# Kernel optimization log

Measured on AMD Instinct MI355X. Metric: run time of the kernel, lower is better.

## Reference

```python
import jax, jax.numpy as jnp
import numpy as np

IN_SZ = 256
OUT_SZ = 256
N_CHAN = 1024
RANK = 4  # min(4, IN_SZ*OUT_SZ)
B = 256
N = 2048


def setup_inputs() -> dict:
    key = jax.random.key(0)
    k_x, k_idx, k_u, k_v, k_b = jax.random.split(key, 5)
    x = jax.random.normal(k_x, (B, N, IN_SZ), dtype=jnp.float32)
    indices = jax.random.randint(k_idx, (B,), 0, N_CHAN)
    # init per reset_parameters(const=1.0)
    bound_u = np.sqrt(3.0 / RANK)              # fan_out of weights_U [C, r] is r
    weights_U = jax.random.uniform(k_u, (N_CHAN, RANK), jnp.float32, -bound_u, bound_u)
    bound_v = np.sqrt(1.0 / (IN_SZ * OUT_SZ))  # fan_out of weights_V [r, in*out]
    weights_V = jax.random.uniform(k_v, (RANK, IN_SZ * OUT_SZ), jnp.float32, -bound_v, bound_v)
    bound_b = np.sqrt(1.0 / RANK)
    bias = jax.random.uniform(k_b, (N_CHAN, 1, OUT_SZ), jnp.float32, -bound_b, bound_b)
    return {"x": x, "indices": indices, "weights_U": weights_U,
            "weights_V": weights_V, "bias": bias}


def reference(x, indices, weights_U, weights_V, bias):
    # weight synthesis: gather U rows first, then low-rank expand (same math as
    # full (U@V)[indices], without materializing unused channels)
    w = (weights_U[indices] @ weights_V).reshape(-1, IN_SZ, OUT_SZ)  # [B, in, out]
    out = jnp.einsum('bni,bio->bno', x, w)                            # [B, N, out]
    out = out + bias[indices]                                         # [B,1,out] broadcast
    return out
```

## Files before the change

kernel.cpp:

```cpp
#include <hip/hip_runtime.h>
#include <cstdint>

#define AS1 __attribute__((address_space(1)))
#define AS3 __attribute__((address_space(3)))

typedef __attribute__((ext_vector_type(8))) short short8;
typedef __attribute__((ext_vector_type(4))) float f32x4;

constexpr int SEQ   = 2048;
constexpr int INSZ  = 256;
constexpr int OUTSZ = 256;

__device__ __forceinline__ ushort f2bf(float f) {
  union { float f; uint32_t u; } v; v.f = f;
  uint32_t u = v.u;
  return (ushort)((u + 0x7FFFu + ((u >> 16) & 1u)) >> 16);
}
__device__ __forceinline__ uint32_t pk2(float a, float b) {
  return (uint32_t)f2bf(a) | ((uint32_t)f2bf(b) << 16);
}
__device__ __forceinline__ uint32_t cvtpk(float lo, float hi) {
  uint32_t r;
  asm("v_cvt_pk_bf16_f32 %0, %1, %2" : "=v"(r) : "v"(lo), "v"(hi));
  return r;
}

__global__ __launch_bounds__(256) void synth_w(
    const float* __restrict__ U, const float* __restrict__ V,
    const int* __restrict__ idx, ushort* __restrict__ wsW)
{
  const int b   = blockIdx.y;
  const int kb  = blockIdx.x;
  const int tid = threadIdx.x;
  const int ch  = idx[b];
  const float u0 = U[ch*4+0], u1 = U[ch*4+1], u2 = U[ch*4+2], u3 = U[ch*4+3];

  __shared__ ushort tile[64][260];

  const int o4    = (tid & 63) * 4;
  const int kbase = (tid >> 6) * 16;
  for (int kk = 0; kk < 16; ++kk) {
    const int k  = kbase + kk;
    const int gk = kb*64 + k;
    const float* vp = V + (size_t)gk*OUTSZ + o4;
    float4 a = *(const float4*)(vp);
    float4 c = *(const float4*)(vp + 65536);
    float4 d = *(const float4*)(vp + 131072);
    float4 e = *(const float4*)(vp + 196608);
    ushort4 pkv;
    pkv.x = f2bf(u0*a.x + u1*c.x + u2*d.x + u3*e.x);
    pkv.y = f2bf(u0*a.y + u1*c.y + u2*d.y + u3*e.y);
    pkv.z = f2bf(u0*a.z + u1*c.z + u2*d.z + u3*e.z);
    pkv.w = f2bf(u0*a.w + u1*c.w + u2*d.w + u3*e.w);
    *(ushort4*)(&tile[k][o4]) = pkv;
  }
  __syncthreads();

  for (int s = 0; s < 8; ++s) {
    const int c      = s*256 + tid;
    const int kshalf = c >> 10;
    const int nb     = (c >> 6) & 15;
    const int lane   = c & 63;
    const int o      = nb*16 + (lane & 15);
    const int k0     = kshalf*32 + (lane >> 4)*8;
    uint4 pkv;
    pkv.x = (uint32_t)tile[k0+0][o] | ((uint32_t)tile[k0+1][o] << 16);
    pkv.y = (uint32_t)tile[k0+2][o] | ((uint32_t)tile[k0+3][o] << 16);
    pkv.z = (uint32_t)tile[k0+4][o] | ((uint32_t)tile[k0+5][o] << 16);
    pkv.w = (uint32_t)tile[k0+6][o] | ((uint32_t)tile[k0+7][o] << 16);
    uint4* dst = (uint4*)(wsW + (size_t)b*65536 + (size_t)(2*kb + kshalf)*8192
                              + nb*512 + lane*8);
    *dst = pkv;
  }
}

__global__ __launch_bounds__(256, 4) void lr_gemm(
    const float* __restrict__ x, const int* __restrict__ idx,
    const float* __restrict__ bias, const ushort* __restrict__ wsW,
    float* __restrict__ out)
{
  __shared__ float ldsF[4][64*32];

  const int wg  = blockIdx.x;
  const int swz = (wg & 7) * 1024 + (wg >> 3);
  const int b   = swz >> 5;
  const int n0  = (swz & 31) * 64;

  const int tid  = threadIdx.x;
  const int lane = tid & 63;
  const int wave = tid >> 6;
  const int hi16 = lane >> 4;
  const int lo16 = lane & 15;

  const float*  xb  = x + ((size_t)b*SEQ + n0)*INSZ;
  const ushort* wbp = wsW + (size_t)b*65536 + wave*2048 + lane*8;

  const int csrc = (lane & 7) ^ (lane >> 3);
#define STAGE(S) do {                                                        \
    _Pragma("unroll")                                                        \
    for (int t = 0; t < 2; ++t) {                                            \
      const int g = wave*2 + t;                        \
      const int r = g*8 + (lane >> 3);                                       \
      const float* srcp = xb + (size_t)r*INSZ + (S)*32 + csrc*4;             \
      float* dstp = &ldsF[(S) & 3][g*256];                                   \
      __builtin_amdgcn_global_load_lds((const AS1 void*)srcp,                \
                                       (AS3 void*)dstp, 16, 0, 0);           \
    } } while (0)

  STAGE(0); STAGE(1); STAGE(2);
  asm volatile("s_waitcnt vmcnt(4)" ::: "memory");
  __builtin_amdgcn_s_barrier();
  __builtin_amdgcn_sched_barrier(0);

  f32x4 acc[4][4] = {};
  const int s0idx = (hi16*2) ^ (lo16 & 7);
  const int s1idx = s0idx ^ 1;

#define KSTEP(S, WSTR) do {                                                  \
    short8 bf[4], af[4];                                                     \
    _Pragma("unroll")                                                        \
    for (int n = 0; n < 4; ++n)                                              \
      bf[n] = *(const short8*)(wbp + (size_t)(S)*8192 + n*512);              \
    if ((S) < 5) STAGE((S)+3);                                               \
    const float* fb = &ldsF[(S) & 3][0];                                     \
    _Pragma("unroll")                                                        \
    for (int m = 0; m < 4; ++m) {                                            \
      const float* p = fb + (m*16 + lo16)*32;                                \
      float4 fa = *(const float4*)(p + s0idx*4);                             \
      float4 fc = *(const float4*)(p + s1idx*4);                             \
      union { uint32_t u[4]; short8 s8; } pk;                                \
      pk.u[0] = cvtpk(fa.x, fa.y); pk.u[1] = cvtpk(fa.z, fa.w);              \
      pk.u[2] = cvtpk(fc.x, fc.y); pk.u[3] = cvtpk(fc.z, fc.w);              \
      af[m] = pk.s8;                                                         \
    }                                                                        \
    _Pragma("unroll")                                                        \
    for (int m = 0; m < 4; ++m)                                              \
      _Pragma("unroll")                                                      \
      for (int n = 0; n < 4; ++n)                                            \
        acc[m][n] = __builtin_amdgcn_mfma_f32_16x16x32_bf16(                 \
            bf[n], af[m], acc[m][n], 0, 0, 0);                               \
    if ((S) < 7) {                                                           \
      __builtin_amdgcn_sched_barrier(0);                                     \
      asm volatile("s_waitcnt vmcnt(" WSTR ")" ::: "memory");                \
      __builtin_amdgcn_s_barrier();                                          \
      __builtin_amdgcn_sched_barrier(0);                                     \
    } } while (0)

  KSTEP(0, "4"); KSTEP(1, "4"); KSTEP(2, "4"); KSTEP(3, "4");
  KSTEP(4, "4"); KSTEP(5, "2"); KSTEP(6, "0"); KSTEP(7, "0");

  const int ch = idx[b];
  float* outb = out + ((size_t)b*SEQ + n0)*OUTSZ;
  #pragma unroll
  for (int n = 0; n < 4; ++n) {
    const float4 bv4 = *(const float4*)(bias + (size_t)ch*OUTSZ
                                        + wave*64 + n*16 + hi16*4);
    #pragma unroll
    for (int m = 0; m < 4; ++m) {
      float4 v;
      v.x = acc[m][n][0] + bv4.x;
      v.y = acc[m][n][1] + bv4.y;
      v.z = acc[m][n][2] + bv4.z;
      v.w = acc[m][n][3] + bv4.w;
      *(float4*)(outb + (size_t)(m*16 + lo16)*OUTSZ
                 + wave*64 + n*16 + hi16*4) = v;
    }
  }
#undef KSTEP
#undef STAGE
}

extern "C" void kernel_launch(void* const* d_in, const int* in_sizes, int n_in,
                              void* d_out, int out_size, void* d_ws, size_t ws_size,
                              hipStream_t stream) {
  const float* x    = (const float*)d_in[0];
  const int*   idx  = (const int*)d_in[1];
  const float* U    = (const float*)d_in[2];
  const float* V    = (const float*)d_in[3];
  const float* bias = (const float*)d_in[4];
  float* out  = (float*)d_out;
  ushort* wsW = (ushort*)d_ws;

  synth_w<<<dim3(4, 256), 256, 0, stream>>>(U, V, idx, wsW);
  lr_gemm<<<8192, 256, 0, stream>>>(x, idx, bias, wsW, out);
}
```

Measured before the change: 255.7 us.

## Deepen GEMM prefetch pipeline with 8 LDS stages and rotating B registers

The lr_gemm kernel now gives each of the 8 K-steps its own LDS buffer (64 KB total) and issues six x-tile stages up front instead of three. The bf16 weight fragments are loaded three steps ahead into four rotating register sets, with vmcnt thresholds retuned to match. The goal is to hide more global-load latency behind MFMA work. In exchange, occupancy drops: launch bounds go from 4 to 2 blocks per CU, and the larger LDS and register footprint limits resident waves.

Measured after the change: 260.2 us. Within noise of the previous version (+1.8%).

```diff
diff --git a/kernel.cpp b/kernel.cpp
--- a/kernel.cpp
+++ b/kernel.cpp
@@ -74,12 +74,12 @@
   }
 }
 
-__global__ __launch_bounds__(256, 4) void lr_gemm(
+__global__ __launch_bounds__(256, 2) void lr_gemm(
     const float* __restrict__ x, const int* __restrict__ idx,
     const float* __restrict__ bias, const ushort* __restrict__ wsW,
     float* __restrict__ out)
 {
-  __shared__ float ldsF[4][64*32];
+  __shared__ float ldsF[8][2048];
 
   const int wg  = blockIdx.x;
   const int swz = (wg & 7) * 1024 + (wg >> 3);
@@ -102,13 +102,23 @@
       const int g = wave*2 + t;                        \
       const int r = g*8 + (lane >> 3);                                       \
       const float* srcp = xb + (size_t)r*INSZ + (S)*32 + csrc*4;             \
-      float* dstp = &ldsF[(S) & 3][g*256];                                   \
+      float* dstp = &ldsF[(S)][g*256];                                       \
       __builtin_amdgcn_global_load_lds((const AS1 void*)srcp,                \
                                        (AS3 void*)dstp, 16, 0, 0);           \
     } } while (0)
 
-  STAGE(0); STAGE(1); STAGE(2);
-  asm volatile("s_waitcnt vmcnt(4)" ::: "memory");
+#define LOADB(DST, S) do {                                                   \
+    _Pragma("unroll")                                                        \
+    for (int n = 0; n < 4; ++n)                                              \
+      DST[n] = *(const short8*)(wbp + (size_t)(S)*8192 + n*512);             \
+    } while (0)
+
+  short8 bfA[4], bfB[4], bfC[4];
+  short8 bfD[4];
+
+  LOADB(bfA, 0); LOADB(bfB, 1); LOADB(bfC, 2);
+  STAGE(0); STAGE(1); STAGE(2); STAGE(3); STAGE(4); STAGE(5);
+  asm volatile("s_waitcnt vmcnt(10)" ::: "memory");
   __builtin_amdgcn_s_barrier();
   __builtin_amdgcn_sched_barrier(0);
 
@@ -116,13 +126,11 @@
   const int s0idx = (hi16*2) ^ (lo16 & 7);
   const int s1idx = s0idx ^ 1;
 
-#define KSTEP(S, WSTR) do {                                                  \
-    short8 bf[4], af[4];                                                     \
-    _Pragma("unroll")                                                        \
-    for (int n = 0; n < 4; ++n)                                              \
-      bf[n] = *(const short8*)(wbp + (size_t)(S)*8192 + n*512);              \
-    if ((S) < 5) STAGE((S)+3);                                               \
-    const float* fb = &ldsF[(S) & 3][0];                                     \
+#define KSTEP(S, BCUR, BLD, DO_LB, DO_ST, DO_FENCE, WSTR) do {               \
+    if (DO_LB) LOADB(BLD, (S)+3);                                            \
+    if (DO_ST) STAGE((S)+6);                                                 \
+    short8 af[4];                                                            \
+    const float* fb = &ldsF[(S)][0];                                         \
     _Pragma("unroll")                                                        \
     for (int m = 0; m < 4; ++m) {                                            \
       const float* p = fb + (m*16 + lo16)*32;                                \
@@ -138,16 +146,22 @@
       _Pragma("unroll")                                                      \
       for (int n = 0; n < 4; ++n)                                            \
         acc[m][n] = __builtin_amdgcn_mfma_f32_16x16x32_bf16(                 \
-            bf[n], af[m], acc[m][n], 0, 0, 0);                               \
-    if ((S) < 7) {                                                           \
+            BCUR[n], af[m], acc[m][n], 0, 0, 0);                             \
+    if (DO_FENCE) {                                                          \
       __builtin_amdgcn_sched_barrier(0);                                     \
       asm volatile("s_waitcnt vmcnt(" WSTR ")" ::: "memory");                \
       __builtin_amdgcn_s_barrier();                                          \
       __builtin_amdgcn_sched_barrier(0);                                     \
     } } while (0)
 
-  KSTEP(0, "4"); KSTEP(1, "4"); KSTEP(2, "4"); KSTEP(3, "4");
-  KSTEP(4, "4"); KSTEP(5, "2"); KSTEP(6, "0"); KSTEP(7, "0");
+  KSTEP(0, bfA, bfD, 1, 1, 1, "14");
+  KSTEP(1, bfB, bfA, 1, 1, 1, "18");
+  KSTEP(2, bfC, bfB, 1, 0, 1, "12");
+  KSTEP(3, bfD, bfC, 1, 0, 1, "10");
+  KSTEP(4, bfA, bfD, 1, 0, 1, "8");
+  KSTEP(5, bfB, bfA, 0, 0, 1, "4");
+  KSTEP(6, bfC, bfA, 0, 0, 1, "0");
+  KSTEP(7, bfD, bfA, 0, 0, 0, "0");
 
   const int ch = idx[b];
   float* outb = out + ((size_t)b*SEQ + n0)*OUTSZ;
@@ -162,11 +176,11 @@
       v.y = acc[m][n][1] + bv4.y;
       v.z = acc[m][n][2] + bv4.z;
       v.w = acc[m][n][3] + bv4.w;
-      *(float4*)(outb + (size_t)(m*16 + lo16)*OUTSZ
-                 + wave*64 + n*16 + hi16*4) = v;
+      *(float4*)(outb + (size_t)(m*16 + lo16)*OUTSZ + wave*64 + n*16 + hi16*4) = v;
     }
   }
 #undef KSTEP
+#undef LOADB
 #undef STAGE
 }
 
```
